# Optimization experiments

Measured on AMD Instinct MI355X. Metric: run time of the kernel, lower is better.

Reference implementation:

```python
import math
import jax, jax.numpy as jnp
import numpy as np

TREE_DEPTH = 4
NUM_NODES = (1 << TREE_DEPTH) - 1  # 15
TAU_MEM = 0.95
TAU_SYN = 0.95
LN_EPS = 1e-5


def _forward(x, W_proj, threshold, node_weights, gamma, beta):
    B, T, D = x.shape
    padded_T = 1 << math.ceil(math.log2(T))
    x_p = jnp.pad(x, ((0, 0), (0, padded_T - T), (0, 0))) if padded_T > T else x

    eff_depth = min(TREE_DEPTH, int(math.log2(padded_T)))
    num_leaves = 1 << eff_depth
    sub_seq = padded_T // num_leaves
    # leaf states: mean over each contiguous chunk -> [B, num_leaves, D]
    leaves = x_p.reshape(B, num_leaves, sub_seq, D).mean(axis=2)

    leaf_start = (1 << (eff_depth - 1)) - 1
    valid_leaves = min(num_leaves, NUM_NODES - leaf_start)
    node_states = jnp.zeros((B, NUM_NODES, D), x.dtype)
    node_states = node_states.at[:, leaf_start:leaf_start + valid_leaves].set(
        leaves[:, :valid_leaves])

    # LIF membrane/synapse buffers, carried across levels within this forward
    v = jnp.zeros((1, 1, D), x.dtype)
    s = jnp.zeros((1, 1, D), x.dtype)

    # bottom-up tree message passing (static, unrolled: eff_depth levels)
    for level in range(eff_depth - 1, -1, -1):
        level_start = (1 << level) - 1
        level_end = min((1 << (level + 1)) - 1, NUM_NODES)
        nodes = np.arange(level_start, level_end)
        left = 2 * nodes + 1
        right = 2 * nodes + 2
        mask = left < NUM_NODES
        if not mask.any():
            continue  # leaf level: children out of range
        nv, lv, rv = nodes[mask], left[mask], right[mask]
        l_st = node_states[:, lv]   # [B, n, D]
        r_st = node_states[:, rv]   # [B, n, D] (full tree -> rv always valid)
        fused = jnp.concatenate([l_st, r_st], axis=-1)  # [B, n, 2D]
        proj = jnp.einsum('bnk,dk->bnd', fused, W_proj)

        # LIF neuron (training-mode math: surrogate * hard spike)
        s_new = TAU_SYN * s + proj                      # broadcast [B,n,D]
        v_new = TAU_MEM * v + s_new - jax.lax.stop_gradient(s_new)
        spike = (v_new >= threshold).astype(x.dtype)
        v_after = v_new - spike * threshold
        surrogate = jax.nn.sigmoid(25.0 * (v_after - threshold))
        spike_out = surrogate * spike
        v = jax.lax.stop_gradient(v_after.mean(axis=(0, 1), keepdims=True))
        s = jax.lax.stop_gradient(s_new.mean(axis=(0, 1), keepdims=True))

        gated = proj * spike_out
        node_states = node_states.at[:, nv].set(gated)

    # per-dim softmax mixture over the 15 tree nodes
    weights = jax.nn.softmax(node_weights, axis=0)             # [N, D]
    mixture = jnp.einsum('nd,bnd->bd', weights, node_states)   # [B, D]

    out = mixture[:, None, :] + x                              # residual, [B,T,D]
    mu = out.mean(axis=-1, keepdims=True)
    var = out.var(axis=-1, keepdims=True)
    out = (out - mu) / jnp.sqrt(var + LN_EPS) * gamma + beta
    return out


def setup_inputs() -> dict:
    key = jax.random.key(0)
    k0, k1, k2 = jax.random.split(key, 3)
    B, T, D = 8, 4096, 1024
    x = jax.random.normal(k0, (B, T, D), dtype=jnp.float32)
    # nn.Linear(2D, D, bias=False): weight [D, 2D]
    W_proj = jax.random.normal(k1, (D, 2 * D), dtype=jnp.float32) / np.sqrt(2 * D).astype(np.float32)
    threshold = jnp.ones((D,), dtype=jnp.float32)        # LIF init: ones
    node_weights = 0.02 * jax.random.normal(k2, (NUM_NODES, D), dtype=jnp.float32)
    gamma = jnp.ones((D,), dtype=jnp.float32)
    beta = jnp.zeros((D,), dtype=jnp.float32)
    return {"x": x, "W_proj": W_proj, "threshold": threshold,
            "node_weights": node_weights, "gamma": gamma, "beta": beta}


def reference(x, W_proj, threshold, node_weights, gamma, beta):
    return _forward(x, W_proj, threshold, node_weights, gamma, beta)
```

## Files before the change

### kernel.cpp

```cpp
#include <hip/hip_runtime.h>

#define Bq 8
#define Tq 4096
#define Dq 1024
#define NLEAF 8
#define SUBSEQ 256
#define TSPLIT 8
#define NNODES 15

typedef float f32x4 __attribute__((ext_vector_type(4)));

__global__ __launch_bounds__(256) void k_leaf_partial(const float* __restrict__ x,
                                                      float* __restrict__ partial) {
    const int bl = blockIdx.x;
    const int p  = blockIdx.y;
    const int q  = threadIdx.x;
    const int b = bl >> 3, l = bl & 7;
    const float4* xp = (const float4*)(x + ((size_t)b * Tq + (size_t)l * SUBSEQ + (size_t)p * (SUBSEQ / TSPLIT)) * Dq) + q;
    float4 s = {0.f, 0.f, 0.f, 0.f};
#pragma unroll 8
    for (int t = 0; t < SUBSEQ / TSPLIT; ++t) {
        float4 xv = xp[(size_t)t * (Dq / 4)];
        s.x += xv.x; s.y += xv.y; s.z += xv.z; s.w += xv.w;
    }
    ((float4*)partial)[((size_t)bl * TSPLIT + p) * (Dq / 4) + q] = s;
}

__global__ __launch_bounds__(1024) void k_mixture(const float* __restrict__ partial,
                                                  const float* __restrict__ nw,
                                                  float* __restrict__ mixture) {
    const int b = blockIdx.x;
    const int d = threadIdx.x;
    float v[NNODES];
    float m = -1e30f;
#pragma unroll
    for (int n = 0; n < NNODES; ++n) {
        v[n] = nw[n * Dq + d];
        m = fmaxf(m, v[n]);
    }
    float denom = 0.f;
#pragma unroll
    for (int n = 0; n < NNODES; ++n) {
        v[n] = expf(v[n] - m);
        denom += v[n];
    }
    const float inv_denom = 1.0f / denom;
    float acc = 0.f;
#pragma unroll
    for (int l = 0; l < NLEAF; ++l) {
        float s = 0.f;
#pragma unroll
        for (int p = 0; p < TSPLIT; ++p)
            s += partial[(((size_t)(b * NLEAF + l)) * TSPLIT + p) * Dq + d];
        const float leaf = s * (1.0f / (float)SUBSEQ);
        acc += (v[7 + l] * inv_denom) * leaf;
    }
    mixture[b * Dq + d] = acc;
}

__global__ __launch_bounds__(256) void k_ln(const float* __restrict__ x,
                                            const float* __restrict__ mixture,
                                            const float* __restrict__ gamma,
                                            const float* __restrict__ beta,
                                            float* __restrict__ out) {
    const int wid  = threadIdx.x >> 6;
    const int lane = threadIdx.x & 63;
    const int row  = blockIdx.x * 4 + wid;
    const int b    = row >> 12;
    const float4* xr = (const float4*)(x + (size_t)row * Dq);
    const float4* mr = (const float4*)(mixture + (size_t)b * Dq);
    float4 o[4];
    float sum = 0.f, sq = 0.f;
#pragma unroll
    for (int k = 0; k < 4; ++k) {
        const float4 xv = xr[lane + 64 * k];
        const float4 mv = mr[lane + 64 * k];
        o[k].x = xv.x + mv.x;
        o[k].y = xv.y + mv.y;
        o[k].z = xv.z + mv.z;
        o[k].w = xv.w + mv.w;
        sum += o[k].x + o[k].y + o[k].z + o[k].w;
        sq  += o[k].x * o[k].x + o[k].y * o[k].y + o[k].z * o[k].z + o[k].w * o[k].w;
    }
#pragma unroll
    for (int i = 32; i >= 1; i >>= 1) {
        sum += __shfl_xor(sum, i, 64);
        sq  += __shfl_xor(sq, i, 64);
    }
    const float mu   = sum * (1.0f / 1024.0f);
    const float var  = sq * (1.0f / 1024.0f) - mu * mu;
    const float rstd = rsqrtf(var + 1e-5f);
    f32x4* orow = (f32x4*)(out + (size_t)row * Dq);
#pragma unroll
    for (int k = 0; k < 4; ++k) {
        const float4 gv = ((const float4*)gamma)[lane + 64 * k];
        const float4 bv = ((const float4*)beta)[lane + 64 * k];
        f32x4 r;
        r.x = (o[k].x - mu) * rstd * gv.x + bv.x;
        r.y = (o[k].y - mu) * rstd * gv.y + bv.y;
        r.z = (o[k].z - mu) * rstd * gv.z + bv.z;
        r.w = (o[k].w - mu) * rstd * gv.w + bv.w;
        __builtin_nontemporal_store(r, &orow[lane + 64 * k]);
    }
}

extern "C" void kernel_launch(void* const* d_in, const int* in_sizes, int n_in,
                              void* d_out, int out_size, void* d_ws, size_t ws_size,
                              hipStream_t stream) {
    const float* x     = (const float*)d_in[0];
    const float* nw    = (const float*)d_in[3];
    const float* gamma = (const float*)d_in[4];
    const float* beta  = (const float*)d_in[5];
    float* out = (float*)d_out;

    float* partial = (float*)d_ws;
    float* mixture = partial + (size_t)Bq * NLEAF * TSPLIT * Dq;

    k_leaf_partial<<<dim3(Bq * NLEAF, TSPLIT), 256, 0, stream>>>(x, partial);
    k_mixture<<<Bq, 1024, 0, stream>>>(partial, nw, mixture);
    k_ln<<<Bq * Tq / 4, 256, 0, stream>>>(x, mixture, gamma, beta, out);
}
```

Before: 59.38 us.

## Fuse leaf reduction and softmax mixture into one kernel with atomic accumulation

Merges the partial leaf-sum kernel and the mixture kernel into one kernel. Each block computes the softmax node weights itself and atomically adds its weighted partial sum into a zeroed mixture buffer. The time split is doubled to 16 for more blocks. This removes one launch and the round trip through a partial buffer, at the cost of a memset, float atomics with nondeterministic summation order, and softmax work repeated in every block.

```diff
diff --git a/kernel.cpp b/kernel.cpp
--- a/kernel.cpp
+++ b/kernel.cpp
@@ -5,57 +5,48 @@
 #define Dq 1024
 #define NLEAF 8
 #define SUBSEQ 256
-#define TSPLIT 8
+#define TSPLIT 16
 #define NNODES 15
 
 typedef float f32x4 __attribute__((ext_vector_type(4)));
 
-__global__ __launch_bounds__(256) void k_leaf_partial(const float* __restrict__ x,
-                                                      float* __restrict__ partial) {
+__global__ __launch_bounds__(256) void k_leaf_fused(const float* __restrict__ x,
+                                                    const float* __restrict__ nw,
+                                                    float* __restrict__ mixture) {
     const int bl = blockIdx.x;
     const int p  = blockIdx.y;
     const int q  = threadIdx.x;
     const int b = bl >> 3, l = bl & 7;
     const float4* xp = (const float4*)(x + ((size_t)b * Tq + (size_t)l * SUBSEQ + (size_t)p * (SUBSEQ / TSPLIT)) * Dq) + q;
     float4 s = {0.f, 0.f, 0.f, 0.f};
-#pragma unroll 8
+#pragma unroll
     for (int t = 0; t < SUBSEQ / TSPLIT; ++t) {
         float4 xv = xp[(size_t)t * (Dq / 4)];
         s.x += xv.x; s.y += xv.y; s.z += xv.z; s.w += xv.w;
     }
-    ((float4*)partial)[((size_t)bl * TSPLIT + p) * (Dq / 4) + q] = s;
-}
-
-__global__ __launch_bounds__(1024) void k_mixture(const float* __restrict__ partial,
-                                                  const float* __restrict__ nw,
-                                                  float* __restrict__ mixture) {
-    const int b = blockIdx.x;
-    const int d = threadIdx.x;
-    float v[NNODES];
-    float m = -1e30f;
+    float4 v[NNODES];
+    float4 m = {-1e30f, -1e30f, -1e30f, -1e30f};
 #pragma unroll
     for (int n = 0; n < NNODES; ++n) {
-        v[n] = nw[n * Dq + d];
-        m = fmaxf(m, v[n]);
+        v[n] = ((const float4*)(nw + n * Dq))[q];
+        m.x = fmaxf(m.x, v[n].x); m.y = fmaxf(m.y, v[n].y);
+        m.z = fmaxf(m.z, v[n].z); m.w = fmaxf(m.w, v[n].w);
     }
-    float denom = 0.f;
+    float4 den = {0.f, 0.f, 0.f, 0.f};
 #pragma unroll
     for (int n = 0; n < NNODES; ++n) {
-        v[n] = expf(v[n] - m);
-        denom += v[n];
+        v[n].x = expf(v[n].x - m.x); den.x += v[n].x;
+        v[n].y = expf(v[n].y - m.y); den.y += v[n].y;
+        v[n].z = expf(v[n].z - m.z); den.z += v[n].z;
+        v[n].w = expf(v[n].w - m.w); den.w += v[n].w;
     }
-    const float inv_denom = 1.0f / denom;
-    float acc = 0.f;
-#pragma unroll
-    for (int l = 0; l < NLEAF; ++l) {
-        float s = 0.f;
-#pragma unroll
-        for (int p = 0; p < TSPLIT; ++p)
-            s += partial[(((size_t)(b * NLEAF + l)) * TSPLIT + p) * Dq + d];
-        const float leaf = s * (1.0f / (float)SUBSEQ);
-        acc += (v[7 + l] * inv_denom) * leaf;
-    }
-    mixture[b * Dq + d] = acc;
+    const float4 wl = v[7 + l];
+    const float c = 1.0f / (float)SUBSEQ;
+    float* mb = mixture + (size_t)b * Dq + 4 * q;
+    atomicAdd(mb + 0, s.x * (wl.x / den.x) * c);
+    atomicAdd(mb + 1, s.y * (wl.y / den.y) * c);
+    atomicAdd(mb + 2, s.z * (wl.z / den.z) * c);
+    atomicAdd(mb + 3, s.w * (wl.w / den.w) * c);
 }
 
 __global__ __launch_bounds__(256) void k_ln(const float* __restrict__ x,
@@ -113,10 +104,9 @@
     const float* beta  = (const float*)d_in[5];
     float* out = (float*)d_out;
 
-    float* partial = (float*)d_ws;
-    float* mixture = partial + (size_t)Bq * NLEAF * TSPLIT * Dq;
+    float* mixture = (float*)d_ws;
 
-    k_leaf_partial<<<dim3(Bq * NLEAF, TSPLIT), 256, 0, stream>>>(x, partial);
-    k_mixture<<<Bq, 1024, 0, stream>>>(partial, nw, mixture);
+    hipMemsetAsync(mixture, 0, (size_t)Bq * Dq * sizeof(float), stream);
+    k_leaf_fused<<<dim3(Bq * NLEAF, TSPLIT), 256, 0, stream>>>(x, nw, mixture);
     k_ln<<<Bq * Tq / 4, 256, 0, stream>>>(x, mixture, gamma, beta, out);
 }
```

New measurement: 90.55 us. 1.52x slower.

## Fuse leaf-sum, mixture and layernorm into one cooperative kernel with register reuse

Applied to the files above, without the earlier changes.

Replaces the three-kernel pipeline with a single cooperative kernel. Each wave keeps its first-half rows of x in registers, reduces them to per-block leaf partials, and grid-syncs so that 16 blocks can compute the softmax-weighted mixture. After a second grid sync, the kernel applies residual plus layernorm to the held rows and then streams the second half of x. This avoids reading the first half of x twice and removes two kernel launches. The cost is two grid-wide barriers, heavy register use for the held rows, and a fixed 512-block grid that may limit occupancy. The old three-kernel path remains as a fallback.

```diff
diff --git a/kernel.cpp b/kernel.cpp
--- a/kernel.cpp
+++ b/kernel.cpp
@@ -1,14 +1,168 @@
 #include <hip/hip_runtime.h>
+#include <hip/hip_cooperative_groups.h>
+
+namespace cg = cooperative_groups;
 
 #define Bq 8
 #define Tq 4096
 #define Dq 1024
-#define NLEAF 8
+#define HALF 2048
+#define NNODES 15
 #define SUBSEQ 256
 #define TSPLIT 8
-#define NNODES 15
+#define CGRID 512
+#define CBLOCK 512
 
 typedef float f32x4 __attribute__((ext_vector_type(4)));
+
+__global__ __launch_bounds__(CBLOCK, 4) void k_fused(
+    const float* __restrict__ x, const float* __restrict__ nw,
+    const float* __restrict__ gamma, const float* __restrict__ beta,
+    float* __restrict__ partial, float* __restrict__ mixture,
+    float* __restrict__ out)
+{
+    const int tid  = threadIdx.x;
+    const int wid  = tid >> 6;
+    const int lane = tid & 63;
+    const int blk  = blockIdx.x;
+    const int fbase = blk * 32 + wid * 4;
+    const int b  = fbase >> 11;
+    const int t0 = fbase & 2047;
+
+    const float4* xr = (const float4*)(x + ((size_t)b * Tq + t0) * Dq);
+    float4 h[4][4];
+    float4 s[4] = {{0,0,0,0},{0,0,0,0},{0,0,0,0},{0,0,0,0}};
+#pragma unroll
+    for (int r = 0; r < 4; ++r)
+#pragma unroll
+        for (int k = 0; k < 4; ++k) {
+            h[r][k] = xr[(size_t)r * 256 + lane + 64 * k];
+            s[k].x += h[r][k].x; s[k].y += h[r][k].y;
+            s[k].z += h[r][k].z; s[k].w += h[r][k].w;
+        }
+    __shared__ float4 ldsv[8][256];
+#pragma unroll
+    for (int k = 0; k < 4; ++k) ldsv[wid][lane + 64 * k] = s[k];
+    __syncthreads();
+    if (tid < 256) {
+        float4 a = ldsv[0][tid];
+#pragma unroll
+        for (int w = 1; w < 8; ++w) {
+            a.x += ldsv[w][tid].x; a.y += ldsv[w][tid].y;
+            a.z += ldsv[w][tid].z; a.w += ldsv[w][tid].w;
+        }
+        ((float4*)partial)[(size_t)blk * 256 + tid] = a;
+    }
+    cg::this_grid().sync();
+
+    if (blk < 16) {
+        const int b2 = blk >> 1;
+        const int d  = ((blk & 1) << 9) + tid;
+        float v[NNODES];
+        float m = -1e30f;
+#pragma unroll
+        for (int n = 0; n < NNODES; ++n) {
+            v[n] = nw[n * Dq + d];
+            m = fmaxf(m, v[n]);
+        }
+        float denom = 0.f;
+#pragma unroll
+        for (int n = 0; n < NNODES; ++n) {
+            v[n] = expf(v[n] - m);
+            denom += v[n];
+        }
+        const float inv_denom = 1.0f / denom;
+        float acc = 0.f;
+#pragma unroll
+        for (int l = 0; l < 8; ++l) {
+            float ls = 0.f;
+#pragma unroll
+            for (int j = 0; j < 8; ++j)
+                ls += partial[(size_t)((b2 * 64 + l * 8 + j) << 10) + d];
+            acc += (v[7 + l] * inv_denom) * (ls * (1.0f / 256.0f));
+        }
+        mixture[b2 * Dq + d] = acc;
+    }
+    cg::this_grid().sync();
+
+    const float4* mr = (const float4*)(mixture + (size_t)b * Dq);
+    const float4* gp = (const float4*)gamma;
+    const float4* bp = (const float4*)beta;
+
+#pragma unroll
+    for (int r = 0; r < 4; ++r) {
+        float4 o[4];
+        float sum = 0.f, sq = 0.f;
+#pragma unroll
+        for (int k = 0; k < 4; ++k) {
+            const float4 mv = mr[lane + 64 * k];
+            o[k].x = h[r][k].x + mv.x;
+            o[k].y = h[r][k].y + mv.y;
+            o[k].z = h[r][k].z + mv.z;
+            o[k].w = h[r][k].w + mv.w;
+            sum += o[k].x + o[k].y + o[k].z + o[k].w;
+            sq  += o[k].x * o[k].x + o[k].y * o[k].y + o[k].z * o[k].z + o[k].w * o[k].w;
+        }
+#pragma unroll
+        for (int i = 32; i >= 1; i >>= 1) {
+            sum += __shfl_xor(sum, i, 64);
+            sq  += __shfl_xor(sq, i, 64);
+        }
+        const float mu   = sum * (1.0f / 1024.0f);
+        const float var  = sq * (1.0f / 1024.0f) - mu * mu;
+        const float rstd = rsqrtf(var + 1e-5f);
+        f32x4* orow = (f32x4*)(out + ((size_t)b * Tq + t0 + r) * Dq);
+#pragma unroll
+        for (int k = 0; k < 4; ++k) {
+            const float4 gv = gp[lane + 64 * k];
+            const float4 bv = bp[lane + 64 * k];
+            f32x4 rr;
+            rr.x = (o[k].x - mu) * rstd * gv.x + bv.x;
+            rr.y = (o[k].y - mu) * rstd * gv.y + bv.y;
+            rr.z = (o[k].z - mu) * rstd * gv.z + bv.z;
+            rr.w = (o[k].w - mu) * rstd * gv.w + bv.w;
+            __builtin_nontemporal_store(rr, &orow[lane + 64 * k]);
+        }
+    }
+
+    const float4* xf = (const float4*)(x + ((size_t)b * Tq + HALF + t0) * Dq);
+#pragma unroll
+    for (int r = 0; r < 4; ++r) {
+        float4 o[4];
+        float sum = 0.f, sq = 0.f;
+#pragma unroll
+        for (int k = 0; k < 4; ++k) {
+            const float4 xv = xf[(size_t)r * 256 + lane + 64 * k];
+            const float4 mv = mr[lane + 64 * k];
+            o[k].x = xv.x + mv.x;
+            o[k].y = xv.y + mv.y;
+            o[k].z = xv.z + mv.z;
+            o[k].w = xv.w + mv.w;
+            sum += o[k].x + o[k].y + o[k].z + o[k].w;
+            sq  += o[k].x * o[k].x + o[k].y * o[k].y + o[k].z * o[k].z + o[k].w * o[k].w;
+        }
+#pragma unroll
+        for (int i = 32; i >= 1; i >>= 1) {
+            sum += __shfl_xor(sum, i, 64);
+            sq  += __shfl_xor(sq, i, 64);
+        }
+        const float mu   = sum * (1.0f / 1024.0f);
+        const float var  = sq * (1.0f / 1024.0f) - mu * mu;
+        const float rstd = rsqrtf(var + 1e-5f);
+        f32x4* orow = (f32x4*)(out + ((size_t)b * Tq + HALF + t0 + r) * Dq);
+#pragma unroll
+        for (int k = 0; k < 4; ++k) {
+            const float4 gv = gp[lane + 64 * k];
+            const float4 bv = bp[lane + 64 * k];
+            f32x4 rr;
+            rr.x = (o[k].x - mu) * rstd * gv.x + bv.x;
+            rr.y = (o[k].y - mu) * rstd * gv.y + bv.y;
+            rr.z = (o[k].z - mu) * rstd * gv.z + bv.z;
+            rr.w = (o[k].w - mu) * rstd * gv.w + bv.w;
+            __builtin_nontemporal_store(rr, &orow[lane + 64 * k]);
+        }
+    }
+}
 
 __global__ __launch_bounds__(256) void k_leaf_partial(const float* __restrict__ x,
                                                       float* __restrict__ partial) {
@@ -47,13 +201,12 @@
     const float inv_denom = 1.0f / denom;
     float acc = 0.f;
 #pragma unroll
-    for (int l = 0; l < NLEAF; ++l) {
+    for (int l = 0; l < 8; ++l) {
         float s = 0.f;
 #pragma unroll
         for (int p = 0; p < TSPLIT; ++p)
-            s += partial[(((size_t)(b * NLEAF + l)) * TSPLIT + p) * Dq + d];
-        const float leaf = s * (1.0f / (float)SUBSEQ);
-        acc += (v[7 + l] * inv_denom) * leaf;
+            s += partial[(((size_t)(b * 8 + l)) * TSPLIT + p) * Dq + d];
+        acc += (v[7 + l] * inv_denom) * (s * (1.0f / (float)SUBSEQ));
     }
     mixture[b * Dq + d] = acc;
 }
@@ -114,9 +267,25 @@
     float* out = (float*)d_out;
 
     float* partial = (float*)d_ws;
-    float* mixture = partial + (size_t)Bq * NLEAF * TSPLIT * Dq;
-
-    k_leaf_partial<<<dim3(Bq * NLEAF, TSPLIT), 256, 0, stream>>>(x, partial);
+    float* mixture = partial + (size_t)CGRID * Dq;
+
+    int dev = 0;
+    hipGetDevice(&dev);
+    int ncu = 0;
+    hipDeviceGetAttribute(&ncu, hipDeviceAttributeMultiprocessorCount, dev);
+    int nb = 0;
+    hipError_t eq = hipOccupancyMaxActiveBlocksPerMultiprocessor(&nb, (const void*)k_fused, CBLOCK, 0);
+    bool coop = (eq == hipSuccess) && ((long)nb * ncu >= CGRID);
+
+    if (coop) {
+        void* args[] = {(void*)&x, (void*)&nw, (void*)&gamma, (void*)&beta,
+                        (void*)&partial, (void*)&mixture, (void*)&out};
+        hipError_t el = hipLaunchCooperativeKernel((void*)k_fused, dim3(CGRID), dim3(CBLOCK),
+                                                   args, 0, stream);
+        if (el == hipSuccess) return;
+    }
+
+    k_leaf_partial<<<dim3(Bq * 8, TSPLIT), 256, 0, stream>>>(x, partial);
     k_mixture<<<Bq, 1024, 0, stream>>>(partial, nw, mixture);
     k_ln<<<Bq * Tq / 4, 256, 0, stream>>>(x, mixture, gamma, beta, out);
 }
```

Measured after the change: 59.41 us. No clear change (+0.0%).
